# Kernel tuning notes

Measured on AMD Instinct MI355X. Metric: run time of the kernel, lower is better.

The kernel has to match this reference:

```python
import jax, jax.numpy as jnp
import numpy as np

P_DROP = 0.1
KEEP = 1.0 - P_DROP


def setup_inputs() -> dict:
    key = jax.random.key(0)
    k1, k2, k3 = jax.random.split(key, 3)
    x1 = jax.random.normal(k1, (32, 512, 768), dtype=jnp.float32)
    x2 = jax.random.normal(k2, (32, 511, 768), dtype=jnp.float32)
    # dropout keep-mask (True = keep), Bernoulli(p_keep=0.9)
    drop_mask = jax.random.bernoulli(k3, KEEP, (32, 512, 511))
    return {"x1": x1, "x2": x2, "drop_mask": drop_mask}


def reference(x1, x2, drop_mask):
    # scores: [b, q, k] = x1 @ x2^T (scale factor is 1 in the original)
    scores = jnp.einsum("bqd,bkd->bqk", x1, x2)
    attn = jax.nn.softmax(scores, axis=-1)
    # inverted dropout with explicit mask: keep/KEEP, drop->0
    attn = jnp.where(drop_mask, attn * (1.0 / KEEP), 0.0)
    # output: [b, q, d] = attn @ x2 (x2 doubles as values)
    return jnp.einsum("bqk,bkd->bqd", attn, x2)
```

## Files before the change

### kernel.cpp

```cpp
#include <hip/hip_runtime.h>


namespace {

constexpr int NB = 32, NQ = 512, NK = 511, ND = 768;
constexpr int TQ = 64, NTH = 512;
constexpr int NCH = 24;
constexpr int NKC = 16;
constexpr float INV_KEEP = 1.0f / 0.9f;

constexpr int BUF0   = 0;
constexpr int BUF1   = 73728;
constexpr int X1H_O  = 0;
constexpr int X1L_O  = 4096;
constexpr int X2H_O  = 8192;
constexpr int X2L_O  = 40960;
constexpr int P_OFF  = 0;
constexpr int VT0    = 65536;
constexpr int VT1    = 114688;
constexpr int RED_OFF = 150528;
constexpr int MLD_OFF = RED_OFF + 2048;
constexpr int FLD_OFF = MLD_OFF + 256;
constexpr int LDS_TOTAL = 163840;

typedef short s8v   __attribute__((ext_vector_type(8)));
typedef float f32x4 __attribute__((ext_vector_type(4)));

__device__ __forceinline__ unsigned f2bf(float x) {
    unsigned u = __float_as_uint(x);
    return (u + 0x7FFFu + ((u >> 16) & 1u)) >> 16;
}
__device__ __forceinline__ unsigned pk_hi(float a, float b) {
    return f2bf(a) | (f2bf(b) << 16);
}
__device__ __forceinline__ void split2(float a, float b, unsigned& hi, unsigned& lo) {
    unsigned ha = f2bf(a), hb = f2bf(b);
    float ra = a - __uint_as_float(ha << 16);
    float rb = b - __uint_as_float(hb << 16);
    hi = ha | (hb << 16);
    lo = (__float_as_uint(ra) >> 16) | ((__float_as_uint(rb) >> 16) << 16);
}

__global__ __launch_bounds__(NTH, 2)
void fused_attn(const float* __restrict__ x1, const float* __restrict__ x2,
                const int* __restrict__ dmask, float* __restrict__ out)
{
    extern __shared__ char smem[];
    const int t  = threadIdx.x;
    const int w  = t >> 6;
    const int l  = t & 63;
    const int li = l & 15;
    const int g  = l >> 4;

    const int logical = ((blockIdx.x & 7) << 5) | (blockIdx.x >> 3);
    const int b  = logical >> 3;
    const int q0 = (logical & 7) * TQ;

    const float* x1b = x1 + (size_t)(b * NQ + q0) * ND;
    const float* x2b = x2 + (size_t)b * NK * ND;
    const int*   mb  = dmask + (size_t)(b * NQ + q0) * NK;
    float*       ob  = out + (size_t)(b * NQ + q0) * ND;

    float* redp = (float*)(smem + RED_OFF);
    float* mldp = (float*)(smem + MLD_OFF);
    float* fldp = (float*)(smem + FLD_OFF);

    f32x4 acc[4][4] = {};

    f32x4 px1;
    f32x4 pxa[4], pxb[4];
    const int r0 = t >> 2, gq1 = t & 3;

    auto loadStage = [&](int dc) {
        const int d0 = dc * 32;
        px1 = *(const f32x4*)(x1b + (size_t)(t >> 3) * ND + d0 + (t & 7) * 4);
        #pragma unroll
        for (int j = 0; j < 4; ++j) {
            const int r = r0 + 128 * j;
            if (r < NK) {
                pxa[j] = *(const f32x4*)(x2b + (size_t)r * ND + d0 + gq1 * 8);
                pxb[j] = *(const f32x4*)(x2b + (size_t)r * ND + d0 + gq1 * 8 + 4);
            } else {
                pxa[j] = (f32x4){0.f, 0.f, 0.f, 0.f};
                pxb[j] = (f32x4){0.f, 0.f, 0.f, 0.f};
            }
        }
    };
    auto writeStage = [&](char* bb) {
        {
            unsigned h0, l0_, h1, l1_;
            split2(px1[0], px1[1], h0, l0_);
            split2(px1[2], px1[3], h1, l1_);
            const int q = t >> 3, cg = t & 7;
            const int a = (q >> 4) * 1024 + ((cg >> 1) * 16 + (q & 15)) * 16 + (cg & 1) * 8;
            *(uint2*)(bb + X1H_O + a) = make_uint2(h0, h1);
            *(uint2*)(bb + X1L_O + a) = make_uint2(l0_, l1_);
        }
        #pragma unroll
        for (int j = 0; j < 4; ++j) {
            const int r = r0 + 128 * j;
            unsigned hh[4], ll[4];
            split2(pxa[j][0], pxa[j][1], hh[0], ll[0]);
            split2(pxa[j][2], pxa[j][3], hh[1], ll[1]);
            split2(pxb[j][0], pxb[j][1], hh[2], ll[2]);
            split2(pxb[j][2], pxb[j][3], hh[3], ll[3]);
            const int a = (r >> 4) * 1024 + (gq1 * 16 + (r & 15)) * 16;
            *(uint4*)(bb + X2H_O + a) = make_uint4(hh[0], hh[1], hh[2], hh[3]);
            *(uint4*)(bb + X2L_O + a) = make_uint4(ll[0], ll[1], ll[2], ll[3]);
        }
    };

    loadStage(0);
    writeStage(smem + BUF0);
    loadStage(1);
    __syncthreads();

    for (int dc = 0; dc < NCH; ++dc) {
        char* cb = smem + ((dc & 1) ? BUF1 : BUF0);
        char* nb = smem + ((dc & 1) ? BUF0 : BUF1);
        if (dc + 1 < NCH) writeStage(nb);
        if (dc + 2 < NCH) loadStage(dc + 2);

        s8v ah[4], al[4], bh[4], bl[4];
        #pragma unroll
        for (int i = 0; i < 4; ++i) {
            ah[i] = *(const s8v*)(cb + X1H_O + i * 1024 + l * 16);
            al[i] = *(const s8v*)(cb + X1L_O + i * 1024 + l * 16);
            bh[i] = *(const s8v*)(cb + X2H_O + (w * 4 + i) * 1024 + l * 16);
            bl[i] = *(const s8v*)(cb + X2L_O + (w * 4 + i) * 1024 + l * 16);
        }
        #pragma unroll
        for (int qb = 0; qb < 4; ++qb)
            #pragma unroll
            for (int c = 0; c < 4; ++c) {
                acc[qb][c] = __builtin_amdgcn_mfma_f32_16x16x32_bf16(ah[qb], bh[c], acc[qb][c], 0, 0, 0);
                acc[qb][c] = __builtin_amdgcn_mfma_f32_16x16x32_bf16(ah[qb], bl[c], acc[qb][c], 0, 0, 0);
                acc[qb][c] = __builtin_amdgcn_mfma_f32_16x16x32_bf16(al[qb], bh[c], acc[qb][c], 0, 0, 0);
            }
        __syncthreads();
    }

    if (w == 7 && li == 15) {
        #pragma unroll
        for (int qb = 0; qb < 4; ++qb)
            #pragma unroll
            for (int r = 0; r < 4; ++r) acc[qb][3][r] = -3.0e38f;
    }
    #pragma unroll
    for (int qb = 0; qb < 4; ++qb)
        #pragma unroll
        for (int r = 0; r < 4; ++r) {
            float v = fmaxf(fmaxf(acc[qb][0][r], acc[qb][1][r]),
                            fmaxf(acc[qb][2][r], acc[qb][3][r]));
            v = fmaxf(v, __shfl_xor(v, 1));
            v = fmaxf(v, __shfl_xor(v, 2));
            v = fmaxf(v, __shfl_xor(v, 4));
            v = fmaxf(v, __shfl_xor(v, 8));
            if (li == 0) redp[(qb * 16 + g * 4 + r) * 8 + w] = v;
        }
    __syncthreads();
    if (t < 64) {
        float v = redp[t * 8];
        #pragma unroll
        for (int i = 1; i < 8; ++i) v = fmaxf(v, redp[t * 8 + i]);
        mldp[t] = v;
    }
    __syncthreads();
    #pragma unroll
    for (int qb = 0; qb < 4; ++qb)
        #pragma unroll
        for (int r = 0; r < 4; ++r) {
            const float m = mldp[qb * 16 + g * 4 + r];
            float e0 = __expf(acc[qb][0][r] - m);
            float e1 = __expf(acc[qb][1][r] - m);
            float e2 = __expf(acc[qb][2][r] - m);
            float e3 = __expf(acc[qb][3][r] - m);
            acc[qb][0][r] = e0; acc[qb][1][r] = e1;
            acc[qb][2][r] = e2; acc[qb][3][r] = e3;
            float s = (e0 + e1) + (e2 + e3);
            s += __shfl_xor(s, 1);
            s += __shfl_xor(s, 2);
            s += __shfl_xor(s, 4);
            s += __shfl_xor(s, 8);
            if (li == 0) redp[(qb * 16 + g * 4 + r) * 8 + w] = s;
        }
    __syncthreads();
    if (t < 64) {
        float s = redp[t * 8];
        #pragma unroll
        for (int i = 1; i < 8; ++i) s += redp[t * 8 + i];
        fldp[t] = INV_KEEP / s;
    }
    __syncthreads();

    float fr[4][4];
    #pragma unroll
    for (int qb = 0; qb < 4; ++qb)
        #pragma unroll
        for (int r = 0; r < 4; ++r) fr[qb][r] = fldp[qb * 16 + g * 4 + r];

    #pragma unroll
    for (int qb = 0; qb < 4; ++qb)
        #pragma unroll
        for (int c = 0; c < 4; ++c)
            #pragma unroll
            for (int r = 0; r < 4; ++r) {
                const int q = qb * 16 + g * 4 + r;
                const int k = w * 64 + c * 16 + li;
                float p = 0.f;
                if (k < NK && mb[(size_t)q * NK + k] != 0) p = acc[qb][c][r];
                float po = __shfl_xor(p, 1);
                if ((li & 1) == 0)
                    *(unsigned*)(smem + P_OFF + qb * 16384 + (k >> 5) * 1024 +
                                 ((k >> 3) & 3) * 256 + (q & 15) * 16 + (k & 7) * 2) = pk_hi(p, po);
            }

    f32x4 o[4][6] = {};
    f32x4 va[8], vb[8];
    const int dqA = t >> 2, gqA = t & 3;
    const int dqB = 128 + (t >> 2);

    auto loadV = [&](int kc) {
        const int kbase = kc * 32;
        #pragma unroll
        for (int e = 0; e < 8; ++e) {
            const int k = kbase + gqA * 8 + e;
            va[e] = (k < NK) ? *(const f32x4*)(x2b + (size_t)k * ND + dqA * 4)
                             : (f32x4){0.f, 0.f, 0.f, 0.f};
        }
        if (t < 256) {
            #pragma unroll
            for (int e = 0; e < 8; ++e) {
                const int k = kbase + gqA * 8 + e;
                vb[e] = (k < NK) ? *(const f32x4*)(x2b + (size_t)k * ND + dqB * 4)
                                 : (f32x4){0.f, 0.f, 0.f, 0.f};
            }
        }
    };
    auto writeV = [&](char* vbase) {
        #pragma unroll
        for (int c = 0; c < 4; ++c) {
            const int d = dqA * 4 + c;
            const int wp = d / 96, rem = d - wp * 96;
            const int a = (wp * 6 + (rem >> 4)) * 1024 + gqA * 256 + ((d & 15) ^ gqA) * 16;
            *(uint4*)(vbase + a) = make_uint4(pk_hi(va[0][c], va[1][c]), pk_hi(va[2][c], va[3][c]),
                                              pk_hi(va[4][c], va[5][c]), pk_hi(va[6][c], va[7][c]));
        }
        if (t < 256) {
            #pragma unroll
            for (int c = 0; c < 4; ++c) {
                const int d = dqB * 4 + c;
                const int wp = d / 96, rem = d - wp * 96;
                const int a = (wp * 6 + (rem >> 4)) * 1024 + gqA * 256 + ((d & 15) ^ gqA) * 16;
                *(uint4*)(vbase + a) = make_uint4(pk_hi(vb[0][c], vb[1][c]), pk_hi(vb[2][c], vb[3][c]),
                                                  pk_hi(vb[4][c], vb[5][c]), pk_hi(vb[6][c], vb[7][c]));
            }
        }
    };

    loadV(0);
    writeV(smem + VT0);
    loadV(1);
    __syncthreads();

    for (int kc = 0; kc < NKC; ++kc) {
        char* cv = smem + ((kc & 1) ? VT1 : VT0);
        char* nv = smem + ((kc & 1) ? VT0 : VT1);
        if (kc + 1 < NKC) writeV(nv);
        if (kc + 2 < NKC) loadV(kc + 2);

        s8v pa[4], pb[6];
        #pragma unroll
        for (int qb = 0; qb < 4; ++qb)
            pa[qb] = *(const s8v*)(smem + P_OFF + qb * 16384 + kc * 1024 + l * 16);
        #pragma unroll
        for (int nf = 0; nf < 6; ++nf)
            pb[nf] = *(const s8v*)(cv + (w * 6 + nf) * 1024 + g * 256 + (li ^ g) * 16);
        #pragma unroll
        for (int qb = 0; qb < 4; ++qb)
            #pragma unroll
            for (int nf = 0; nf < 6; ++nf)
                o[qb][nf] = __builtin_amdgcn_mfma_f32_16x16x32_bf16(pa[qb], pb[nf], o[qb][nf], 0, 0, 0);
        __syncthreads();
    }

    #pragma unroll
    for (int qb = 0; qb < 4; ++qb)
        #pragma unroll
        for (int r = 0; r < 4; ++r) {
            const float f = fr[qb][r];
            #pragma unroll
            for (int nf = 0; nf < 6; ++nf)
                ob[(size_t)(qb * 16 + g * 4 + r) * ND + w * 96 + nf * 16 + li] = o[qb][nf][r] * f;
        }
}

}

extern "C" void kernel_launch(void* const* d_in, const int* in_sizes, int n_in,
                              void* d_out, int out_size, void* d_ws, size_t ws_size,
                              hipStream_t stream)
{
    const float* x1    = (const float*)d_in[0];
    const float* x2    = (const float*)d_in[1];
    const int*   dmask = (const int*)d_in[2];
    float*       out   = (float*)d_out;

    (void)hipFuncSetAttribute((const void*)fused_attn,
                              hipFuncAttributeMaxDynamicSharedMemorySize, LDS_TOTAL);
    fused_attn<<<dim3(NB * (NQ / TQ)), dim3(NTH), LDS_TOTAL, stream>>>(x1, x2, dmask, out);
}
```

Measured before the change: 278.5 us.

## Halve query tile and block size, split K and D passes, add LDS swizzles

Shrinks the query tile from 64 to 32 rows and the block from 512 to 256 threads. The QK^T phase is split into two key-halves per d-chunk and the PV phase into two 384-wide D halves, which roughly halves LDS use so more blocks fit per CU. It also adds XOR swizzles to the LDS layouts to reduce bank conflicts and switches bf16 packing to the hardware conversion intrinsic. In exchange, x2 is re-read from global memory for twice as many blocks, and the MFMA work per LDS load is lower.

```diff
diff --git a/kernel.cpp b/kernel.cpp
--- a/kernel.cpp
+++ b/kernel.cpp
@@ -1,45 +1,40 @@
 #include <hip/hip_runtime.h>
+#include <hip/hip_bf16.h>
 
 
 namespace {
 
 constexpr int NB = 32, NQ = 512, NK = 511, ND = 768;
-constexpr int TQ = 64, NTH = 512;
-constexpr int NCH = 24;
-constexpr int NKC = 16;
+constexpr int TQ = 32, NTH = 256;
+constexpr int NST = 48;
+constexpr int NTAU = 32;
 constexpr float INV_KEEP = 1.0f / 0.9f;
 
-constexpr int BUF0   = 0;
-constexpr int BUF1   = 73728;
-constexpr int X1H_O  = 0;
-constexpr int X1L_O  = 4096;
-constexpr int X2H_O  = 8192;
-constexpr int X2L_O  = 40960;
-constexpr int P_OFF  = 0;
-constexpr int VT0    = 65536;
-constexpr int VT1    = 114688;
-constexpr int RED_OFF = 150528;
-constexpr int MLD_OFF = RED_OFF + 2048;
-constexpr int FLD_OFF = MLD_OFF + 256;
-constexpr int LDS_TOTAL = 163840;
+constexpr int X2H_O = 0;
+constexpr int X2L_O = 16384;
+constexpr int X1REG = 65536;
+constexpr int P_OFF = 0;
+constexpr int VT0   = 32768;
+constexpr int VT1   = 57344;
+constexpr int RED_OFF = 73728;
+constexpr int MLD_OFF = 74240;
+constexpr int FLD_OFF = 74368;
+constexpr int LDS_TOTAL = 81920;
 
 typedef short s8v   __attribute__((ext_vector_type(8)));
 typedef float f32x4 __attribute__((ext_vector_type(4)));
 
-__device__ __forceinline__ unsigned f2bf(float x) {
-    unsigned u = __float_as_uint(x);
-    return (u + 0x7FFFu + ((u >> 16) & 1u)) >> 16;
-}
-__device__ __forceinline__ unsigned pk_hi(float a, float b) {
-    return f2bf(a) | (f2bf(b) << 16);
+__device__ __forceinline__ unsigned pk2(float a, float b) {
+    __hip_bfloat162 h = __float22bfloat162_rn(make_float2(a, b));
+    unsigned u; __builtin_memcpy(&u, &h, 4); return u;
 }
 __device__ __forceinline__ void split2(float a, float b, unsigned& hi, unsigned& lo) {
-    unsigned ha = f2bf(a), hb = f2bf(b);
-    float ra = a - __uint_as_float(ha << 16);
-    float rb = b - __uint_as_float(hb << 16);
-    hi = ha | (hb << 16);
-    lo = (__float_as_uint(ra) >> 16) | ((__float_as_uint(rb) >> 16) << 16);
-}
+    hi = pk2(a, b);
+    float ra = a - __uint_as_float(hi << 16);
+    float rb = b - __uint_as_float(hi & 0xffff0000u);
+    lo = pk2(ra, rb);
+}
+__device__ __forceinline__ constexpr int SW(int g) { return (5 * g) & 15; }
 
 __global__ __launch_bounds__(NTH, 2)
 void fused_attn(const float* __restrict__ x1, const float* __restrict__ x2,
@@ -52,9 +47,9 @@
     const int li = l & 15;
     const int g  = l >> 4;
 
-    const int logical = ((blockIdx.x & 7) << 5) | (blockIdx.x >> 3);
-    const int b  = logical >> 3;
-    const int q0 = (logical & 7) * TQ;
+    const int logical = ((blockIdx.x & 7) << 6) | (blockIdx.x >> 3);
+    const int b  = logical >> 4;
+    const int q0 = (logical & 15) * TQ;
 
     const float* x1b = x1 + (size_t)(b * NQ + q0) * ND;
     const float* x2b = x2 + (size_t)b * NK * ND;
@@ -65,234 +60,254 @@
     float* mldp = (float*)(smem + MLD_OFF);
     float* fldp = (float*)(smem + FLD_OFF);
 
-    f32x4 acc[4][4] = {};
+    f32x4 acc[2][8] = {};
 
     f32x4 px1;
     f32x4 pxa[4], pxb[4];
-    const int r0 = t >> 2, gq1 = t & 3;
-
-    auto loadStage = [&](int dc) {
-        const int d0 = dc * 32;
-        px1 = *(const f32x4*)(x1b + (size_t)(t >> 3) * ND + d0 + (t & 7) * 4);
+    const int r0 = t >> 2, gq = t & 3;
+
+    auto loadStage = [&](int st) {
+        const int d0 = (st >> 1) * 32;
+        const int kh = (st & 1) * 256;
+        if ((st & 1) == 0)
+            px1 = *(const f32x4*)(x1b + (size_t)(t >> 3) * ND + d0 + (t & 7) * 4);
         #pragma unroll
         for (int j = 0; j < 4; ++j) {
-            const int r = r0 + 128 * j;
-            if (r < NK) {
-                pxa[j] = *(const f32x4*)(x2b + (size_t)r * ND + d0 + gq1 * 8);
-                pxb[j] = *(const f32x4*)(x2b + (size_t)r * ND + d0 + gq1 * 8 + 4);
+            const int kr = kh + r0 + 64 * j;
+            if (kr < NK) {
+                pxa[j] = *(const f32x4*)(x2b + (size_t)kr * ND + d0 + gq * 8);
+                pxb[j] = *(const f32x4*)(x2b + (size_t)kr * ND + d0 + gq * 8 + 4);
             } else {
                 pxa[j] = (f32x4){0.f, 0.f, 0.f, 0.f};
                 pxb[j] = (f32x4){0.f, 0.f, 0.f, 0.f};
             }
         }
     };
-    auto writeStage = [&](char* bb) {
-        {
-            unsigned h0, l0_, h1, l1_;
-            split2(px1[0], px1[1], h0, l0_);
-            split2(px1[2], px1[3], h1, l1_);
-            const int q = t >> 3, cg = t & 7;
-            const int a = (q >> 4) * 1024 + ((cg >> 1) * 16 + (q & 15)) * 16 + (cg & 1) * 8;
-            *(uint2*)(bb + X1H_O + a) = make_uint2(h0, h1);
-            *(uint2*)(bb + X1L_O + a) = make_uint2(l0_, l1_);
-        }
+    auto writeStage = [&](int st) {
+        char* bb = smem + (st & 1) * 32768;
         #pragma unroll
         for (int j = 0; j < 4; ++j) {
-            const int r = r0 + 128 * j;
+            const int rloc = r0 + 64 * j;
             unsigned hh[4], ll[4];
             split2(pxa[j][0], pxa[j][1], hh[0], ll[0]);
             split2(pxa[j][2], pxa[j][3], hh[1], ll[1]);
             split2(pxb[j][0], pxb[j][1], hh[2], ll[2]);
             split2(pxb[j][2], pxb[j][3], hh[3], ll[3]);
-            const int a = (r >> 4) * 1024 + (gq1 * 16 + (r & 15)) * 16;
+            const int a = (rloc >> 4) * 1024 + (gq * 16 + ((rloc & 15) ^ SW(gq))) * 16;
             *(uint4*)(bb + X2H_O + a) = make_uint4(hh[0], hh[1], hh[2], hh[3]);
             *(uint4*)(bb + X2L_O + a) = make_uint4(ll[0], ll[1], ll[2], ll[3]);
         }
+        if ((st & 1) == 0) {
+            unsigned h0, l0_, h1, l1_;
+            split2(px1[0], px1[1], h0, l0_);
+            split2(px1[2], px1[3], h1, l1_);
+            const int row = t >> 3, dgrp = t & 7, dg2 = dgrp >> 1;
+            char* xb = smem + X1REG + ((st >> 1) & 1) * 4096;
+            const int a = (row >> 4) * 1024 + (dg2 * 16 + ((row & 15) ^ SW(dg2))) * 16 + (dgrp & 1) * 8;
+            *(uint2*)(xb + a)        = make_uint2(h0, h1);
+            *(uint2*)(xb + 2048 + a) = make_uint2(l0_, l1_);
+        }
     };
 
     loadStage(0);
-    writeStage(smem + BUF0);
+    writeStage(0);
     loadStage(1);
     __syncthreads();
 
-    for (int dc = 0; dc < NCH; ++dc) {
-        char* cb = smem + ((dc & 1) ? BUF1 : BUF0);
-        char* nb = smem + ((dc & 1) ? BUF0 : BUF1);
-        if (dc + 1 < NCH) writeStage(nb);
-        if (dc + 2 < NCH) loadStage(dc + 2);
-
-        s8v ah[4], al[4], bh[4], bl[4];
-        #pragma unroll
-        for (int i = 0; i < 4; ++i) {
-            ah[i] = *(const s8v*)(cb + X1H_O + i * 1024 + l * 16);
-            al[i] = *(const s8v*)(cb + X1L_O + i * 1024 + l * 16);
-            bh[i] = *(const s8v*)(cb + X2H_O + (w * 4 + i) * 1024 + l * 16);
-            bl[i] = *(const s8v*)(cb + X2L_O + (w * 4 + i) * 1024 + l * 16);
-        }
-        #pragma unroll
-        for (int qb = 0; qb < 4; ++qb)
+    for (int s = 0; s < NST; ++s) {
+        if (s + 1 < NST) writeStage(s + 1);
+        if (s + 2 < NST) loadStage(s + 2);
+
+        const char* xb1 = smem + X1REG + ((s >> 1) & 1) * 4096;
+        const char* xb2 = smem + (s & 1) * 32768;
+        const int   so  = (g * 16 + (li ^ SW(g))) * 16;
+        s8v ah[2], al[2], bh[4], bl[4];
+        #pragma unroll
+        for (int qb = 0; qb < 2; ++qb) {
+            ah[qb] = *(const s8v*)(xb1 + qb * 1024 + so);
+            al[qb] = *(const s8v*)(xb1 + 2048 + qb * 1024 + so);
+        }
+        #pragma unroll
+        for (int c = 0; c < 4; ++c) {
+            bh[c] = *(const s8v*)(xb2 + X2H_O + (w * 4 + c) * 1024 + so);
+            bl[c] = *(const s8v*)(xb2 + X2L_O + (w * 4 + c) * 1024 + so);
+        }
+        const int cb = (s & 1) * 4;
+        #pragma unroll
+        for (int qb = 0; qb < 2; ++qb)
             #pragma unroll
             for (int c = 0; c < 4; ++c) {
-                acc[qb][c] = __builtin_amdgcn_mfma_f32_16x16x32_bf16(ah[qb], bh[c], acc[qb][c], 0, 0, 0);
-                acc[qb][c] = __builtin_amdgcn_mfma_f32_16x16x32_bf16(ah[qb], bl[c], acc[qb][c], 0, 0, 0);
-                acc[qb][c] = __builtin_amdgcn_mfma_f32_16x16x32_bf16(al[qb], bh[c], acc[qb][c], 0, 0, 0);
+                acc[qb][cb + c] = __builtin_amdgcn_mfma_f32_16x16x32_bf16(ah[qb], bh[c], acc[qb][cb + c], 0, 0, 0);
+                acc[qb][cb + c] = __builtin_amdgcn_mfma_f32_16x16x32_bf16(ah[qb], bl[c], acc[qb][cb + c], 0, 0, 0);
+                acc[qb][cb + c] = __builtin_amdgcn_mfma_f32_16x16x32_bf16(al[qb], bh[c], acc[qb][cb + c], 0, 0, 0);
             }
         __syncthreads();
     }
 
-    if (w == 7 && li == 15) {
-        #pragma unroll
-        for (int qb = 0; qb < 4; ++qb)
-            #pragma unroll
-            for (int r = 0; r < 4; ++r) acc[qb][3][r] = -3.0e38f;
+    if (w == 3 && li == 15) {
+        #pragma unroll
+        for (int qb = 0; qb < 2; ++qb)
+            #pragma unroll
+            for (int r = 0; r < 4; ++r) acc[qb][7][r] = -3.0e38f;
     }
     #pragma unroll
-    for (int qb = 0; qb < 4; ++qb)
+    for (int qb = 0; qb < 2; ++qb)
         #pragma unroll
         for (int r = 0; r < 4; ++r) {
-            float v = fmaxf(fmaxf(acc[qb][0][r], acc[qb][1][r]),
-                            fmaxf(acc[qb][2][r], acc[qb][3][r]));
+            float v = -3.0e38f;
+            #pragma unroll
+            for (int c = 0; c < 8; ++c) v = fmaxf(v, acc[qb][c][r]);
             v = fmaxf(v, __shfl_xor(v, 1));
             v = fmaxf(v, __shfl_xor(v, 2));
             v = fmaxf(v, __shfl_xor(v, 4));
             v = fmaxf(v, __shfl_xor(v, 8));
-            if (li == 0) redp[(qb * 16 + g * 4 + r) * 8 + w] = v;
-        }
-    __syncthreads();
-    if (t < 64) {
-        float v = redp[t * 8];
-        #pragma unroll
-        for (int i = 1; i < 8; ++i) v = fmaxf(v, redp[t * 8 + i]);
+            if (li == 0) redp[(qb * 16 + g * 4 + r) * 4 + w] = v;
+        }
+    __syncthreads();
+    if (t < 32) {
+        float v = fmaxf(fmaxf(redp[t * 4], redp[t * 4 + 1]),
+                        fmaxf(redp[t * 4 + 2], redp[t * 4 + 3]));
         mldp[t] = v;
     }
     __syncthreads();
     #pragma unroll
-    for (int qb = 0; qb < 4; ++qb)
+    for (int qb = 0; qb < 2; ++qb)
         #pragma unroll
         for (int r = 0; r < 4; ++r) {
             const float m = mldp[qb * 16 + g * 4 + r];
-            float e0 = __expf(acc[qb][0][r] - m);
-            float e1 = __expf(acc[qb][1][r] - m);
-            float e2 = __expf(acc[qb][2][r] - m);
-            float e3 = __expf(acc[qb][3][r] - m);
-            acc[qb][0][r] = e0; acc[qb][1][r] = e1;
-            acc[qb][2][r] = e2; acc[qb][3][r] = e3;
-            float s = (e0 + e1) + (e2 + e3);
+            float s = 0.f;
+            #pragma unroll
+            for (int c = 0; c < 8; ++c) {
+                float e = __expf(acc[qb][c][r] - m);
+                acc[qb][c][r] = e;
+                s += e;
+            }
             s += __shfl_xor(s, 1);
             s += __shfl_xor(s, 2);
             s += __shfl_xor(s, 4);
             s += __shfl_xor(s, 8);
-            if (li == 0) redp[(qb * 16 + g * 4 + r) * 8 + w] = s;
-        }
-    __syncthreads();
-    if (t < 64) {
-        float s = redp[t * 8];
-        #pragma unroll
-        for (int i = 1; i < 8; ++i) s += redp[t * 8 + i];
+            if (li == 0) redp[(qb * 16 + g * 4 + r) * 4 + w] = s;
+        }
+    __syncthreads();
+    if (t < 32) {
+        float s = (redp[t * 4] + redp[t * 4 + 1]) + (redp[t * 4 + 2] + redp[t * 4 + 3]);
         fldp[t] = INV_KEEP / s;
     }
     __syncthreads();
 
-    float fr[4][4];
+    float fr[2][4];
     #pragma unroll
-    for (int qb = 0; qb < 4; ++qb)
+    for (int qb = 0; qb < 2; ++qb)
         #pragma unroll
         for (int r = 0; r < 4; ++r) fr[qb][r] = fldp[qb * 16 + g * 4 + r];
 
     #pragma unroll
-    for (int qb = 0; qb < 4; ++qb)
-        #pragma unroll
-        for (int c = 0; c < 4; ++c)
+    for (int qb = 0; qb < 2; ++qb)
+        #pragma unroll
+        for (int c = 0; c < 8; ++c)
             #pragma unroll
             for (int r = 0; r < 4; ++r) {
                 const int q = qb * 16 + g * 4 + r;
-                const int k = w * 64 + c * 16 + li;
+                const int k = (c >> 2) * 256 + w * 64 + (c & 3) * 16 + li;
                 float p = 0.f;
                 if (k < NK && mb[(size_t)q * NK + k] != 0) p = acc[qb][c][r];
                 float po = __shfl_xor(p, 1);
-                if ((li & 1) == 0)
-                    *(unsigned*)(smem + P_OFF + qb * 16384 + (k >> 5) * 1024 +
-                                 ((k >> 3) & 3) * 256 + (q & 15) * 16 + (k & 7) * 2) = pk_hi(p, po);
-            }
-
-    f32x4 o[4][6] = {};
-    f32x4 va[8], vb[8];
-    const int dqA = t >> 2, gqA = t & 3;
-    const int dqB = 128 + (t >> 2);
-
-    auto loadV = [&](int kc) {
-        const int kbase = kc * 32;
+                if ((li & 1) == 0) {
+                    const int ksub = (k >> 3) & 3;
+                    const int a = qb * 16384 + (k >> 5) * 1024 +
+                                  (ksub * 16 + ((q & 15) ^ SW(ksub))) * 16 + (k & 7) * 2;
+                    *(unsigned*)(smem + P_OFF + a) = pk2(p, po);
+                }
+            }
+
+    f32x4 o[2][6] = {};
+    f32x4 va[8], vb2[8];
+    const int dqA = t >> 2;
+
+    auto loadV = [&](int st) {
+        const int dh = st >> 4, kc = st & 15;
+        const int dbase = dh * 384;
         #pragma unroll
         for (int e = 0; e < 8; ++e) {
-            const int k = kbase + gqA * 8 + e;
-            va[e] = (k < NK) ? *(const f32x4*)(x2b + (size_t)k * ND + dqA * 4)
+            const int k = kc * 32 + gq * 8 + e;
+            va[e] = (k < NK) ? *(const f32x4*)(x2b + (size_t)k * ND + dbase + dqA * 4)
                              : (f32x4){0.f, 0.f, 0.f, 0.f};
         }
-        if (t < 256) {
+        if (t < 128) {
             #pragma unroll
             for (int e = 0; e < 8; ++e) {
-                const int k = kbase + gqA * 8 + e;
-                vb[e] = (k < NK) ? *(const f32x4*)(x2b + (size_t)k * ND + dqB * 4)
-                                 : (f32x4){0.f, 0.f, 0.f, 0.f};
-            }
-        }
-    };
-    auto writeV = [&](char* vbase) {
+                const int k = kc * 32 + gq * 8 + e;
+                vb2[e] = (k < NK) ? *(const f32x4*)(x2b + (size_t)k * ND + dbase + (64 + dqA) * 4)
+                                  : (f32x4){0.f, 0.f, 0.f, 0.f};
+            }
+        }
+    };
+    auto writeV = [&](int st) {
+        char* vbase = smem + ((st & 1) ? VT1 : VT0);
         #pragma unroll
         for (int c = 0; c < 4; ++c) {
-            const int d = dqA * 4 + c;
-            const int wp = d / 96, rem = d - wp * 96;
-            const int a = (wp * 6 + (rem >> 4)) * 1024 + gqA * 256 + ((d & 15) ^ gqA) * 16;
-            *(uint4*)(vbase + a) = make_uint4(pk_hi(va[0][c], va[1][c]), pk_hi(va[2][c], va[3][c]),
-                                              pk_hi(va[4][c], va[5][c]), pk_hi(va[6][c], va[7][c]));
-        }
-        if (t < 256) {
+            const int dl = dqA * 4 + c;
+            const int a = (dl >> 4) * 1024 + (gq * 16 + ((dl & 15) ^ SW(gq))) * 16;
+            *(uint4*)(vbase + a) = make_uint4(pk2(va[0][c], va[1][c]), pk2(va[2][c], va[3][c]),
+                                              pk2(va[4][c], va[5][c]), pk2(va[6][c], va[7][c]));
+        }
+        if (t < 128) {
             #pragma unroll
             for (int c = 0; c < 4; ++c) {
-                const int d = dqB * 4 + c;
-                const int wp = d / 96, rem = d - wp * 96;
-                const int a = (wp * 6 + (rem >> 4)) * 1024 + gqA * 256 + ((d & 15) ^ gqA) * 16;
-                *(uint4*)(vbase + a) = make_uint4(pk_hi(vb[0][c], vb[1][c]), pk_hi(vb[2][c], vb[3][c]),
-                                                  pk_hi(vb[4][c], vb[5][c]), pk_hi(vb[6][c], vb[7][c]));
-            }
-        }
+                const int dl = (64 + dqA) * 4 + c;
+                const int a = (dl >> 4) * 1024 + (gq * 16 + ((dl & 15) ^ SW(gq))) * 16;
+                *(uint4*)(vbase + a) = make_uint4(pk2(vb2[0][c], vb2[1][c]), pk2(vb2[2][c], vb2[3][c]),
+                                                  pk2(vb2[4][c], vb2[5][c]), pk2(vb2[6][c], vb2[7][c]));
+            }
+        }
+    };
+    auto storeHalf = [&](int dh) {
+        #pragma unroll
+        for (int qb = 0; qb < 2; ++qb)
+            #pragma unroll
+            for (int r = 0; r < 4; ++r) {
+                const float f = fr[qb][r];
+                #pragma unroll
+                for (int nf = 0; nf < 6; ++nf)
+                    ob[(size_t)(qb * 16 + g * 4 + r) * ND + dh * 384 + w * 96 + nf * 16 + li] =
+                        o[qb][nf][r] * f;
+            }
     };
 
     loadV(0);
-    writeV(smem + VT0);
+    writeV(0);
     loadV(1);
     __syncthreads();
 
-    for (int kc = 0; kc < NKC; ++kc) {
-        char* cv = smem + ((kc & 1) ? VT1 : VT0);
-        char* nv = smem + ((kc & 1) ? VT0 : VT1);
-        if (kc + 1 < NKC) writeV(nv);
-        if (kc + 2 < NKC) loadV(kc + 2);
-
-        s8v pa[4], pb[6];
-        #pragma unroll
-        for (int qb = 0; qb < 4; ++qb)
-            pa[qb] = *(const s8v*)(smem + P_OFF + qb * 16384 + kc * 1024 + l * 16);
+    for (int tau = 0; tau < NTAU; ++tau) {
+        if (tau + 1 < NTAU) writeV(tau + 1);
+        if (tau + 2 < NTAU) loadV(tau + 2);
+
+        const char* cv = smem + ((tau & 1) ? VT1 : VT0);
+        const int   so = (g * 16 + (li ^ SW(g))) * 16;
+        s8v pa[2], pb[6];
+        #pragma unroll
+        for (int qb = 0; qb < 2; ++qb)
+            pa[qb] = *(const s8v*)(smem + P_OFF + qb * 16384 + (tau & 15) * 1024 + so);
         #pragma unroll
         for (int nf = 0; nf < 6; ++nf)
-            pb[nf] = *(const s8v*)(cv + (w * 6 + nf) * 1024 + g * 256 + (li ^ g) * 16);
-        #pragma unroll
-        for (int qb = 0; qb < 4; ++qb)
+            pb[nf] = *(const s8v*)(cv + (w * 6 + nf) * 1024 + so);
+        #pragma unroll
+        for (int qb = 0; qb < 2; ++qb)
             #pragma unroll
             for (int nf = 0; nf < 6; ++nf)
                 o[qb][nf] = __builtin_amdgcn_mfma_f32_16x16x32_bf16(pa[qb], pb[nf], o[qb][nf], 0, 0, 0);
+
+        if (tau == 15) {
+            storeHalf(0);
+            #pragma unroll
+            for (int qb = 0; qb < 2; ++qb)
+                #pragma unroll
+                for (int nf = 0; nf < 6; ++nf) o[qb][nf] = (f32x4){0.f, 0.f, 0.f, 0.f};
+        }
         __syncthreads();
     }
-
-    #pragma unroll
-    for (int qb = 0; qb < 4; ++qb)
-        #pragma unroll
-        for (int r = 0; r < 4; ++r) {
-            const float f = fr[qb][r];
-            #pragma unroll
-            for (int nf = 0; nf < 6; ++nf)
-                ob[(size_t)(qb * 16 + g * 4 + r) * ND + w * 96 + nf * 16 + li] = o[qb][nf][r] * f;
-        }
+    storeHalf(1);
 }
 
 }
```

Result: slower. 692.5 us (+148.6%).
